# Kernel optimization log

Hardware: AMD Instinct MI355X
Metric: run time of the kernel (lower is better)

The kernel has to match this reference:

```python
import jax, jax.numpy as jnp
import numpy as np

WINDOW = (7, 7)
SHIFT = (3, 3)
NUM_HEADS = 4
DIM = 128


def _rel_pos_index():
    wh, ww = WINDOW
    coords = np.stack(np.meshgrid(np.arange(wh), np.arange(ww), indexing='ij'))  # [2,wh,ww]
    cf = coords.reshape(2, -1)                    # [2, N]
    rc = (cf[:, :, None] - cf[:, None, :]).transpose(1, 2, 0)  # [N,N,2]
    rc[:, :, 0] += wh - 1
    rc[:, :, 1] += ww - 1
    rc[:, :, 0] *= 2 * ww - 1
    return jnp.asarray(rc.sum(-1).reshape(-1))    # [N*N] int


def _attn_mask_np(pH, pW, sh):
    # Static-shape shift mask (host-side numpy; constant under jit).
    wh, ww = WINDOW
    m = np.zeros((pH, pW))
    h_slices = ((0, pH - wh), (pH - wh, pH - sh[0]), (pH - sh[0], pH))
    w_slices = ((0, pW - ww), (pW - ww, pW - sh[1]), (pW - sh[1], pW))
    cnt = 0
    for hs in h_slices:
        for ws in w_slices:
            m[hs[0]:hs[1], ws[0]:ws[1]] = cnt
            cnt += 1
    m = m.reshape(pH // wh, wh, pW // ww, ww).transpose(0, 2, 1, 3).reshape(-1, wh * ww)
    diff = m[:, None, :] - m[:, :, None]          # [num_windows, N, N]
    return jnp.asarray(np.where(diff != 0, -100.0, 0.0), dtype=np.float32)


def setup_inputs() -> dict:
    key = jax.random.key(0)
    ks = jax.random.split(key, 9)
    B, H, W, C = 32, 56, 56, DIM
    return {
        'input_q': jax.random.normal(ks[0], (B, H, W, C), jnp.float32),
        'input_k': jax.random.normal(ks[1], (B, H, W, C), jnp.float32),
        'input_v': jax.random.normal(ks[2], (B, H, W, C), jnp.float32),
        'q_weight': jax.random.normal(ks[3], (C, C), jnp.float32) * 0.05,
        'q_bias': jnp.zeros((C,), jnp.float32),
        'k_weight': jax.random.normal(ks[4], (C, C), jnp.float32) * 0.05,
        'k_bias': jnp.zeros((C,), jnp.float32),
        'v_weight': jax.random.normal(ks[5], (C, C), jnp.float32) * 0.05,
        'v_bias': jnp.zeros((C,), jnp.float32),
        'proj_weight': jax.random.normal(ks[6], (C, C), jnp.float32) * 0.05,
        'proj_bias': jnp.zeros((C,), jnp.float32),
        'rpb_table': jax.random.normal(ks[7], ((2 * WINDOW[0] - 1) * (2 * WINDOW[1] - 1), NUM_HEADS), jnp.float32) * 0.02,
    }


def reference(input_q, input_k, input_v, q_weight, q_bias, k_weight, k_bias,
              v_weight, v_bias, proj_weight, proj_bias, rpb_table):
    B, H, W, C = input_q.shape
    wh, ww = WINDOW
    pad_b = (wh - H % wh) % wh
    pad_r = (ww - W % ww) % ww
    pad = lambda t: jnp.pad(t, ((0, 0), (0, pad_b), (0, pad_r), (0, 0)))
    qx, kx, vx = pad(input_q), pad(input_k), pad(input_v)
    pad_H, pad_W = H + pad_b, W + pad_r
    sh = [0 if wh >= pad_H else SHIFT[0], 0 if ww >= pad_W else SHIFT[1]]
    if sum(sh) > 0:
        roll = lambda t: jnp.roll(t, (-sh[0], -sh[1]), axis=(1, 2))
        qx, kx, vx = roll(qx), roll(kx), roll(vx)
    nWh, nWw = pad_H // wh, pad_W // ww
    num_windows = nWh * nWw
    N = wh * ww

    def part(t):  # [B,pH,pW,C] -> [B*num_windows, N, C]
        t = t.reshape(B, nWh, wh, nWw, ww, C).transpose(0, 1, 3, 2, 4, 5)
        return t.reshape(B * num_windows, N, C)

    qx, kx, vx = part(qx), part(kx), part(vx)
    hd = C // NUM_HEADS

    def heads(x, w, b):  # linear + split heads -> [BW, nH, N, hd]
        return (x @ w.T + b).reshape(-1, N, NUM_HEADS, hd).transpose(0, 2, 1, 3)

    q = heads(qx, q_weight, q_bias) * (hd ** -0.5)
    k = heads(kx, k_weight, k_bias)
    v = heads(vx, v_weight, v_bias)

    attn = jnp.einsum('whqd,whkd->whqk', q, k)    # [BW, nH, N, N]
    rpb = rpb_table[_rel_pos_index()].reshape(N, N, NUM_HEADS).transpose(2, 0, 1)[None]
    attn = attn + rpb
    if sum(sh) > 0:
        mask = _attn_mask_np(pad_H, pad_W, sh)    # [num_windows, N, N]
        attn = attn.reshape(B, num_windows, NUM_HEADS, N, N) + mask[None, :, None]
        attn = attn.reshape(B * num_windows, NUM_HEADS, N, N)
    attn = jax.nn.softmax(attn, axis=-1)

    x = jnp.einsum('whqk,whkd->whqd', attn, v).transpose(0, 2, 1, 3).reshape(B * num_windows, N, C)
    x = x @ proj_weight.T + proj_bias
    x = x.reshape(B, nWh, nWw, wh, ww, C).transpose(0, 1, 3, 2, 4, 5).reshape(B, pad_H, pad_W, C)
    if sum(sh) > 0:
        x = jnp.roll(x, (sh[0], sh[1]), axis=(1, 2))
    return x[:, :H, :W, :]
```

## Files before the change

### kernel.cpp

```cpp
#include <hip/hip_runtime.h>
#include <hip/hip_bf16.h>

typedef __attribute__((ext_vector_type(8))) short s16x8;
typedef __attribute__((ext_vector_type(4))) float f32x4;
typedef __attribute__((ext_vector_type(2))) unsigned int u32x2;
typedef __attribute__((ext_vector_type(4))) unsigned int u32x4;

#define MFMA16(a, b, c) __builtin_amdgcn_mfma_f32_16x16x32_bf16((a), (b), (c), 0, 0, 0)
#define LOG2E 1.4426950408889634f

static __device__ __forceinline__ unsigned int pk2(float a, float b) {
  union { __hip_bfloat162 h2; unsigned int u; } cv;
  cv.h2 = __float22bfloat162_rn(make_float2(a, b));
  return cv.u;
}
static __device__ __forceinline__ int div7(int x) { return (x * 9363) >> 16; }
static __device__ __forceinline__ int swz256(int row, int byteoff) {
  return row * 256 + (byteoff ^ ((row & 7) << 4));
}
static __device__ __forceinline__ int swz128(int row, int byteoff) {
  return row * 128 + (byteoff ^ ((row & 7) << 4));
}

__global__ void swin_prep(const float* __restrict__ wq, const float* __restrict__ wk,
                          const float* __restrict__ wv, const float* __restrict__ wp,
                          const float* __restrict__ rpb_table,
                          unsigned short* __restrict__ wsW, float* __restrict__ rpbm) {
  int idx = blockIdx.x * 256 + threadIdx.x;
  if (idx < 65536) {
    int t = idx >> 14, loc = idx & 16383;
    const float* s = (t == 0) ? wq : (t == 1) ? wk : (t == 2) ? wv : wp;
    union { __hip_bfloat16 h; unsigned short u; } cv;
    cv.h = __float2bfloat16(s[loc]);
    wsW[idx] = cv.u;
  } else {
    int k = idx - 65536;
    int c = k >> 14;
    int h = (k >> 12) & 3;
    int i = (k >> 6) & 63, j = k & 63;
    float val;
    if (j >= 49) val = -1e30f;
    else if (i >= 49) val = 0.f;
    else {
      int yi = div7(i), xi = i - yi * 7;
      int yj = div7(j), xj = j - yj * 7;
      int ridx = (yi - yj + 6) * 13 + (xi - xj + 6);
      val = rpb_table[ridx * 4 + h];
      int cwi = c >> 1, cwj = c & 1;
      int rgi = (cwi ? (yi < 4 ? 3 : 6) : 0) + (cwj ? (xi < 4 ? 1 : 2) : 0);
      int rgj = (cwi ? (yj < 4 ? 3 : 6) : 0) + (cwj ? (xj < 4 ? 1 : 2) : 0);
      if (rgi != rgj) val -= 100.f;
      val *= LOG2E;
    }
    rpbm[k] = val;
  }
}

__global__ __launch_bounds__(512, 4) void swin_main(
    const float* __restrict__ xq, const float* __restrict__ xk, const float* __restrict__ xv,
    const float* __restrict__ bq, const float* __restrict__ bk, const float* __restrict__ bv,
    const float* __restrict__ bp, const unsigned short* __restrict__ wsW,
    const float* __restrict__ rpbm, float* __restrict__ out) {
  __shared__ __align__(16) char sm[65536];

  const int tid = threadIdx.x;
  const int lane = tid & 63;
  const int wv_ = tid >> 6;
  const int l15 = lane & 15;
  const int lg = lane >> 4;
  const int kgrp = lg * 8;
  const int rsub = lg * 4;

  const int bid = blockIdx.x;
  const int b = bid >> 6;
  const int widx = bid & 63;
  const int wi = widx >> 3, wj = widx & 7;
  const long obase = (long)b * 56 * 56 * 128;
  const int mcase = ((wi == 7) ? 2 : 0) + ((wj == 7) ? 1 : 0);

  const int xrow = tid >> 3;
  const int xk16 = (tid & 7) << 4;
  long xoff = -1;
  if (xrow < 49) {
    int ty = div7(xrow), tx = xrow - ty * 7;
    int ih = wi * 7 + ty + 3; if (ih >= 56) ih -= 56;
    int iw = wj * 7 + tx + 3; if (iw >= 56) iw -= 56;
    xoff = obase + (long)((ih * 56 + iw) * 128 + xk16);
  }
  float xr[16];
#pragma unroll
  for (int i = 0; i < 16; ++i) xr[i] = 0.f;

  auto issue_x = [&](const float* src) {
    if (xoff >= 0) {
      const float* p = src + xoff;
#pragma unroll
      for (int q = 0; q < 4; ++q) {
        f32x4 v = *(const f32x4*)(p + q * 4);
        xr[q * 4 + 0] = v[0]; xr[q * 4 + 1] = v[1];
        xr[q * 4 + 2] = v[2]; xr[q * 4 + 3] = v[3];
      }
    }
  };
  auto write_x = [&]() {
    unsigned int w[8];
#pragma unroll
    for (int i = 0; i < 8; ++i) w[i] = pk2(xr[2 * i], xr[2 * i + 1]);
    u32x4 a = {w[0], w[1], w[2], w[3]};
    u32x4 bb = {w[4], w[5], w[6], w[7]};
    *(u32x4*)(sm + swz256(xrow, xk16 * 2)) = a;
    *(u32x4*)(sm + swz256(xrow, xk16 * 2 + 16)) = bb;
  };
  auto st2 = [&](int a0, int a1, float v0, float v1) {
    unsigned int u = pk2(v0, v1);
    *(unsigned short*)(sm + a0) = (unsigned short)u;
    *(unsigned short*)(sm + a1) = (unsigned short)(u >> 16);
  };

  auto linearT = [&](int woff, const float* bias, float scale, int dstbase) {
    const int nrow = wv_ * 16 + l15;
    s16x8 afr[4];
#pragma unroll
    for (int kt = 0; kt < 4; ++kt)
      afr[kt] = *(const s16x8*)(wsW + woff + nrow * 128 + kt * 32 + kgrp);
    f32x4 bv4 = *(const f32x4*)(bias + wv_ * 16 + rsub);
    float bb0 = bv4[0] * scale, bb1 = bv4[1] * scale;
    float bb2 = bv4[2] * scale, bb3 = bv4[3] * scale;
#pragma unroll
    for (int tt = 0; tt < 4; ++tt) {
      f32x4 acc = {0.f, 0.f, 0.f, 0.f};
#pragma unroll
      for (int kt = 0; kt < 4; ++kt) {
        s16x8 bfr = *(const s16x8*)(sm + swz256(tt * 16 + l15, (kt * 32 + kgrp) * 2));
        acc = MFMA16(afr[kt], bfr, acc);
      }
      u32x2 pkw = {pk2(acc[0] * scale + bb0, acc[1] * scale + bb1),
                   pk2(acc[2] * scale + bb2, acc[3] * scale + bb3)};
      *(u32x2*)(sm + dstbase + swz256(tt * 16 + l15, 2 * (wv_ * 16 + rsub))) = pkw;
    }
  };

  auto linearV = [&](int woff, const float* bias) {
    const int n = wv_ * 16 + l15;
    s16x8 bfr[4];
#pragma unroll
    for (int kt = 0; kt < 4; ++kt)
      bfr[kt] = *(const s16x8*)(wsW + woff + n * 128 + kt * 32 + kgrp);
    float bval = bias[n];
#pragma unroll
    for (int mt = 0; mt < 4; ++mt) {
      f32x4 acc = {0.f, 0.f, 0.f, 0.f};
#pragma unroll
      for (int kt = 0; kt < 4; ++kt) {
        s16x8 afr = *(const s16x8*)(sm + swz256(mt * 16 + l15, (kt * 32 + kgrp) * 2));
        acc = MFMA16(afr, bfr[kt], acc);
      }
      u32x2 pkw = {pk2(acc[0] + bval, acc[1] + bval), pk2(acc[2] + bval, acc[3] + bval)};
      *(u32x2*)(sm + 49152 + swz128(n, 2 * (mt * 16 + rsub))) = pkw;
    }
  };

  const float QSCALE = 0.17677669529663687f * LOG2E;

  issue_x(xq);
  write_x(); __syncthreads();
  issue_x(xk);
  linearT(0, bq, QSCALE, 16384); __syncthreads();
  write_x(); __syncthreads();
  issue_x(xv);
  linearT(16384, bk, 1.f, 32768); __syncthreads();
  write_x(); __syncthreads();

  const int h = wv_ & 3;
  const int half = wv_ >> 2;
  const int coff = h * 32;
  f32x4 S[2][4];
  {
    linearV(32768, bv);

    const float* rpbm_h = rpbm + (((mcase << 2) + h) << 12);
    float rv[2][4][4];
#pragma unroll
    for (int m2 = 0; m2 < 2; ++m2)
#pragma unroll
      for (int r = 0; r < 4; ++r) {
        int i = (half * 2 + m2) * 16 + rsub + r;
        const float* rp = rpbm_h + i * 64 + l15;
#pragma unroll
        for (int jt = 0; jt < 4; ++jt) rv[m2][jt][r] = rp[jt * 16];
      }

    s16x8 kfr[4];
#pragma unroll
    for (int jt = 0; jt < 4; ++jt)
      kfr[jt] = *(const s16x8*)(sm + 32768 + swz256(jt * 16 + l15, (coff + kgrp) * 2));
#pragma unroll
    for (int m2 = 0; m2 < 2; ++m2) {
      int mt = half * 2 + m2;
      s16x8 qfr = *(const s16x8*)(sm + 16384 + swz256(mt * 16 + l15, (coff + kgrp) * 2));
#pragma unroll
      for (int jt = 0; jt < 4; ++jt) {
        f32x4 z = {0.f, 0.f, 0.f, 0.f};
        S[m2][jt] = MFMA16(qfr, kfr[jt], z);
      }
    }

#pragma unroll
    for (int m2 = 0; m2 < 2; ++m2)
#pragma unroll
      for (int jt = 0; jt < 4; ++jt)
#pragma unroll
        for (int r = 0; r < 4; ++r) S[m2][jt][r] += rv[m2][jt][r];

#pragma unroll
    for (int m2 = 0; m2 < 2; ++m2) {
#pragma unroll
      for (int r = 0; r < 4; ++r) {
        float m = fmaxf(fmaxf(S[m2][0][r], S[m2][1][r]), fmaxf(S[m2][2][r], S[m2][3][r]));
        for (int d = 1; d < 16; d <<= 1) m = fmaxf(m, __shfl_xor(m, d));
        float e0 = exp2f(S[m2][0][r] - m);
        float e1 = exp2f(S[m2][1][r] - m);
        float e2 = exp2f(S[m2][2][r] - m);
        float e3 = exp2f(S[m2][3][r] - m);
        float s = e0 + e1 + e2 + e3;
        for (int d = 1; d < 16; d <<= 1) s += __shfl_xor(s, d);
        float inv = 1.0f / s;
        S[m2][0][r] = e0 * inv; S[m2][1][r] = e1 * inv;
        S[m2][2][r] = e2 * inv; S[m2][3][r] = e3 * inv;
      }
    }
  }
  __syncthreads();

  const int pbase = 16384 + h * 8192;
#pragma unroll
  for (int m2 = 0; m2 < 2; ++m2) {
    int i0 = (half * 2 + m2) * 16 + rsub;
#pragma unroll
    for (int jt = 0; jt < 4; ++jt) {
      int bo = 2 * (jt * 16 + l15);
      st2(pbase + swz128(i0, bo), pbase + swz128(i0 + 1, bo), S[m2][jt][0], S[m2][jt][1]);
      st2(pbase + swz128(i0 + 2, bo), pbase + swz128(i0 + 3, bo), S[m2][jt][2], S[m2][jt][3]);
    }
  }
  __syncthreads();

  {
    s16x8 vfr[2][2];
#pragma unroll
    for (int ks = 0; ks < 2; ++ks)
#pragma unroll
      for (int ct = 0; ct < 2; ++ct) {
        int c = coff + ct * 16 + l15;
        vfr[ks][ct] = *(const s16x8*)(sm + 49152 + swz128(c, (ks * 32 + kgrp) * 2));
      }
    f32x4 Oacc[2][2];
#pragma unroll
    for (int ct = 0; ct < 2; ++ct)
#pragma unroll
      for (int qt = 0; qt < 2; ++qt) Oacc[ct][qt] = (f32x4){0.f, 0.f, 0.f, 0.f};
#pragma unroll
    for (int qt = 0; qt < 2; ++qt) {
#pragma unroll
      for (int ks = 0; ks < 2; ++ks) {
        s16x8 pfr = *(const s16x8*)(sm + pbase + swz128((half * 2 + qt) * 16 + l15, (ks * 32 + kgrp) * 2));
        Oacc[0][qt] = MFMA16(vfr[ks][0], pfr, Oacc[0][qt]);
        Oacc[1][qt] = MFMA16(vfr[ks][1], pfr, Oacc[1][qt]);
      }
    }
#pragma unroll
    for (int ct = 0; ct < 2; ++ct)
#pragma unroll
      for (int qt = 0; qt < 2; ++qt) {
        int qtok = (half * 2 + qt) * 16 + l15;
        u32x2 pkw = {pk2(Oacc[ct][qt][0], Oacc[ct][qt][1]),
                     pk2(Oacc[ct][qt][2], Oacc[ct][qt][3])};
        *(u32x2*)(sm + swz256(qtok, 2 * (coff + ct * 16 + rsub))) = pkw;
      }
  }
  __syncthreads();

  {
    const int nrow = wv_ * 16 + l15;
    s16x8 afr[4];
#pragma unroll
    for (int kt = 0; kt < 4; ++kt)
      afr[kt] = *(const s16x8*)(wsW + 49152 + nrow * 128 + kt * 32 + kgrp);
    f32x4 bv4 = *(const f32x4*)(bp + wv_ * 16 + rsub);
#pragma unroll
    for (int tt = 0; tt < 4; ++tt) {
      f32x4 acc = {0.f, 0.f, 0.f, 0.f};
#pragma unroll
      for (int kt = 0; kt < 4; ++kt) {
        s16x8 bfr = *(const s16x8*)(sm + swz256(tt * 16 + l15, (kt * 32 + kgrp) * 2));
        acc = MFMA16(afr[kt], bfr, acc);
      }
      int tok = tt * 16 + l15;
      if (tok < 49) {
        int ty = div7(tok), tx = tok - ty * 7;
        int oh = wi * 7 + ty + 3; if (oh >= 56) oh -= 56;
        int ow = wj * 7 + tx + 3; if (ow >= 56) ow -= 56;
        f32x4 res = {acc[0] + bv4[0], acc[1] + bv4[1], acc[2] + bv4[2], acc[3] + bv4[3]};
        *(f32x4*)(out + obase + (oh * 56 + ow) * 128 + wv_ * 16 + rsub) = res;
      }
    }
  }
}

extern "C" void kernel_launch(void* const* d_in, const int* in_sizes, int n_in,
                              void* d_out, int out_size, void* d_ws, size_t ws_size,
                              hipStream_t stream) {
  const float* xq = (const float*)d_in[0];
  const float* xk = (const float*)d_in[1];
  const float* xv = (const float*)d_in[2];
  const float* wq = (const float*)d_in[3];
  const float* bq = (const float*)d_in[4];
  const float* wk = (const float*)d_in[5];
  const float* bk = (const float*)d_in[6];
  const float* wv = (const float*)d_in[7];
  const float* bv = (const float*)d_in[8];
  const float* wp = (const float*)d_in[9];
  const float* bp = (const float*)d_in[10];
  const float* rpb = (const float*)d_in[11];

  unsigned short* wsW = (unsigned short*)d_ws;
  float* rpbm = (float*)((char*)d_ws + 131072);

  swin_prep<<<512, 256, 0, stream>>>(wq, wk, wv, wp, rpb, wsW, rpbm);

  float* out = (float*)d_out;
  swin_main<<<2048, 512, 0, stream>>>(xq, xk, xv, bq, bk, bv, bp, wsW, rpbm, out);
}
```

Baseline: 81.39 us.

## Use 32x32 MFMA for attention, keep P in registers, shrink LDS

Rewrites the QK^T and PV stages to use 32x32x16 MFMA with transposed S so each lane owns a query row, doing softmax mostly in-lane with one cross-half shuffle. The probabilities stay in registers and are exchanged via shuffles instead of going through LDS. The V projection is moved after the softmax so buffers can be reused, cutting shared memory from 64KB to 48KB and raising the occupancy hint to 6 blocks. This risks extra register pressure and an added barrier reshuffle.

```diff
diff --git a/kernel.cpp b/kernel.cpp
--- a/kernel.cpp
+++ b/kernel.cpp
@@ -3,10 +3,12 @@
 
 typedef __attribute__((ext_vector_type(8))) short s16x8;
 typedef __attribute__((ext_vector_type(4))) float f32x4;
+typedef __attribute__((ext_vector_type(16))) float f32x16;
 typedef __attribute__((ext_vector_type(2))) unsigned int u32x2;
 typedef __attribute__((ext_vector_type(4))) unsigned int u32x4;
 
 #define MFMA16(a, b, c) __builtin_amdgcn_mfma_f32_16x16x32_bf16((a), (b), (c), 0, 0, 0)
+#define MFMA32(a, b, c) __builtin_amdgcn_mfma_f32_32x32x16_bf16((a), (b), (c), 0, 0, 0)
 #define LOG2E 1.4426950408889634f
 
 static __device__ __forceinline__ unsigned int pk2(float a, float b) {
@@ -56,12 +58,12 @@
   }
 }
 
-__global__ __launch_bounds__(512, 4) void swin_main(
+__global__ __launch_bounds__(512, 6) void swin_main(
     const float* __restrict__ xq, const float* __restrict__ xk, const float* __restrict__ xv,
     const float* __restrict__ bq, const float* __restrict__ bk, const float* __restrict__ bv,
     const float* __restrict__ bp, const unsigned short* __restrict__ wsW,
     const float* __restrict__ rpbm, float* __restrict__ out) {
-  __shared__ __align__(16) char sm[65536];
+  __shared__ __align__(16) char sm[49152];
 
   const int tid = threadIdx.x;
   const int lane = tid & 63;
@@ -70,6 +72,8 @@
   const int lg = lane >> 4;
   const int kgrp = lg * 8;
   const int rsub = lg * 4;
+  const int l31 = lane & 31;
+  const int hi = lane >> 5;
 
   const int bid = blockIdx.x;
   const int b = bid >> 6;
@@ -111,11 +115,6 @@
     *(u32x4*)(sm + swz256(xrow, xk16 * 2)) = a;
     *(u32x4*)(sm + swz256(xrow, xk16 * 2 + 16)) = bb;
   };
-  auto st2 = [&](int a0, int a1, float v0, float v1) {
-    unsigned int u = pk2(v0, v1);
-    *(unsigned short*)(sm + a0) = (unsigned short)u;
-    *(unsigned short*)(sm + a1) = (unsigned short)(u >> 16);
-  };
 
   auto linearT = [&](int woff, const float* bias, float scale, int dstbase) {
     const int nrow = wv_ * 16 + l15;
@@ -156,7 +155,7 @@
         acc = MFMA16(afr, bfr[kt], acc);
       }
       u32x2 pkw = {pk2(acc[0] + bval, acc[1] + bval), pk2(acc[2] + bval, acc[3] + bval)};
-      *(u32x2*)(sm + 49152 + swz128(n, 2 * (mt * 16 + rsub))) = pkw;
+      *(u32x2*)(sm + 16384 + swz128(n, 2 * (mt * 16 + rsub))) = pkw;
     }
   };
 
@@ -169,114 +168,80 @@
   write_x(); __syncthreads();
   issue_x(xv);
   linearT(16384, bk, 1.f, 32768); __syncthreads();
-  write_x(); __syncthreads();
+  write_x();
 
   const int h = wv_ & 3;
   const int half = wv_ >> 2;
   const int coff = h * 32;
-  f32x4 S[2][4];
+  unsigned int pu[2][4][2];
   {
-    linearV(32768, bv);
-
-    const float* rpbm_h = rpbm + (((mcase << 2) + h) << 12);
-    float rv[2][4][4];
-#pragma unroll
-    for (int m2 = 0; m2 < 2; ++m2)
-#pragma unroll
-      for (int r = 0; r < 4; ++r) {
-        int i = (half * 2 + m2) * 16 + rsub + r;
-        const float* rp = rpbm_h + i * 64 + l15;
-#pragma unroll
-        for (int jt = 0; jt < 4; ++jt) rv[m2][jt][r] = rp[jt * 16];
-      }
-
-    s16x8 kfr[4];
-#pragma unroll
-    for (int jt = 0; jt < 4; ++jt)
-      kfr[jt] = *(const s16x8*)(sm + 32768 + swz256(jt * 16 + l15, (coff + kgrp) * 2));
-#pragma unroll
-    for (int m2 = 0; m2 < 2; ++m2) {
-      int mt = half * 2 + m2;
-      s16x8 qfr = *(const s16x8*)(sm + 16384 + swz256(mt * 16 + l15, (coff + kgrp) * 2));
-#pragma unroll
-      for (int jt = 0; jt < 4; ++jt) {
-        f32x4 z = {0.f, 0.f, 0.f, 0.f};
-        S[m2][jt] = MFMA16(qfr, kfr[jt], z);
-      }
-    }
-
-#pragma unroll
-    for (int m2 = 0; m2 < 2; ++m2)
-#pragma unroll
-      for (int jt = 0; jt < 4; ++jt)
-#pragma unroll
-        for (int r = 0; r < 4; ++r) S[m2][jt][r] += rv[m2][jt][r];
-
-#pragma unroll
-    for (int m2 = 0; m2 < 2; ++m2) {
-#pragma unroll
-      for (int r = 0; r < 4; ++r) {
-        float m = fmaxf(fmaxf(S[m2][0][r], S[m2][1][r]), fmaxf(S[m2][2][r], S[m2][3][r]));
-        for (int d = 1; d < 16; d <<= 1) m = fmaxf(m, __shfl_xor(m, d));
-        float e0 = exp2f(S[m2][0][r] - m);
-        float e1 = exp2f(S[m2][1][r] - m);
-        float e2 = exp2f(S[m2][2][r] - m);
-        float e3 = exp2f(S[m2][3][r] - m);
-        float s = e0 + e1 + e2 + e3;
-        for (int d = 1; d < 16; d <<= 1) s += __shfl_xor(s, d);
-        float inv = 1.0f / s;
-        S[m2][0][r] = e0 * inv; S[m2][1][r] = e1 * inv;
-        S[m2][2][r] = e2 * inv; S[m2][3][r] = e3 * inv;
-      }
-    }
+    s16x8 qfr[2], kfr[2][2];
+#pragma unroll
+    for (int s = 0; s < 2; ++s) {
+      qfr[s] = *(const s16x8*)(sm + 16384 + swz256(half * 32 + l31, 2 * (coff + s * 16 + hi * 8)));
+#pragma unroll
+      for (int t = 0; t < 2; ++t)
+        kfr[t][s] = *(const s16x8*)(sm + 32768 + swz256(t * 32 + l31, 2 * (coff + s * 16 + hi * 8)));
+    }
+    f32x16 S[2];
+    S[0] = (f32x16)0.f; S[1] = (f32x16)0.f;
+#pragma unroll
+    for (int s = 0; s < 2; ++s) {
+      S[0] = MFMA32(kfr[0][s], qfr[s], S[0]);
+      S[1] = MFMA32(kfr[1][s], qfr[s], S[1]);
+    }
+    const float* rpbm_h = rpbm + (((mcase << 2) + h) << 12) + (half * 32 + l31) * 64 + 4 * hi;
+#pragma unroll
+    for (int t = 0; t < 2; ++t)
+#pragma unroll
+      for (int g = 0; g < 4; ++g) {
+        f32x4 rv = *(const f32x4*)(rpbm_h + t * 32 + g * 8);
+#pragma unroll
+        for (int e = 0; e < 4; ++e) S[t][g * 4 + e] += rv[e];
+      }
+    float m = S[0][0];
+#pragma unroll
+    for (int t = 0; t < 2; ++t)
+#pragma unroll
+      for (int r = 0; r < 16; ++r) m = fmaxf(m, S[t][r]);
+    m = fmaxf(m, __shfl_xor(m, 32));
+    float sum = 0.f;
+#pragma unroll
+    for (int t = 0; t < 2; ++t)
+#pragma unroll
+      for (int r = 0; r < 16; ++r) { float e = exp2f(S[t][r] - m); S[t][r] = e; sum += e; }
+    sum += __shfl_xor(sum, 32);
+    float inv = 1.0f / sum;
+#pragma unroll
+    for (int t = 0; t < 2; ++t)
+#pragma unroll
+      for (int g = 0; g < 4; ++g) {
+        pu[t][g][0] = pk2(S[t][g * 4 + 0] * inv, S[t][g * 4 + 1] * inv);
+        pu[t][g][1] = pk2(S[t][g * 4 + 2] * inv, S[t][g * 4 + 3] * inv);
+      }
   }
   __syncthreads();
-
-  const int pbase = 16384 + h * 8192;
-#pragma unroll
-  for (int m2 = 0; m2 < 2; ++m2) {
-    int i0 = (half * 2 + m2) * 16 + rsub;
-#pragma unroll
-    for (int jt = 0; jt < 4; ++jt) {
-      int bo = 2 * (jt * 16 + l15);
-      st2(pbase + swz128(i0, bo), pbase + swz128(i0 + 1, bo), S[m2][jt][0], S[m2][jt][1]);
-      st2(pbase + swz128(i0 + 2, bo), pbase + swz128(i0 + 3, bo), S[m2][jt][2], S[m2][jt][3]);
-    }
-  }
+  linearV(32768, bv);
   __syncthreads();
 
   {
-    s16x8 vfr[2][2];
-#pragma unroll
-    for (int ks = 0; ks < 2; ++ks)
-#pragma unroll
-      for (int ct = 0; ct < 2; ++ct) {
-        int c = coff + ct * 16 + l15;
-        vfr[ks][ct] = *(const s16x8*)(sm + 49152 + swz128(c, (ks * 32 + kgrp) * 2));
-      }
-    f32x4 Oacc[2][2];
-#pragma unroll
-    for (int ct = 0; ct < 2; ++ct)
-#pragma unroll
-      for (int qt = 0; qt < 2; ++qt) Oacc[ct][qt] = (f32x4){0.f, 0.f, 0.f, 0.f};
-#pragma unroll
-    for (int qt = 0; qt < 2; ++qt) {
-#pragma unroll
-      for (int ks = 0; ks < 2; ++ks) {
-        s16x8 pfr = *(const s16x8*)(sm + pbase + swz128((half * 2 + qt) * 16 + l15, (ks * 32 + kgrp) * 2));
-        Oacc[0][qt] = MFMA16(vfr[ks][0], pfr, Oacc[0][qt]);
-        Oacc[1][qt] = MFMA16(vfr[ks][1], pfr, Oacc[1][qt]);
-      }
-    }
-#pragma unroll
-    for (int ct = 0; ct < 2; ++ct)
-#pragma unroll
-      for (int qt = 0; qt < 2; ++qt) {
-        int qtok = (half * 2 + qt) * 16 + l15;
-        u32x2 pkw = {pk2(Oacc[ct][qt][0], Oacc[ct][qt][1]),
-                     pk2(Oacc[ct][qt][2], Oacc[ct][qt][3])};
-        *(u32x2*)(sm + swz256(qtok, 2 * (coff + ct * 16 + rsub))) = pkw;
-      }
+    f32x16 O = (f32x16)0.f;
+#pragma unroll
+    for (int s = 0; s < 4; ++s) {
+      const int t = s >> 1, gb = (s & 1) * 2;
+      unsigned int own0 = pu[t][gb + hi][0], own1 = pu[t][gb + hi][1];
+      unsigned int po0 = __shfl_xor(pu[t][gb + 1 - hi][0], 32);
+      unsigned int po1 = __shfl_xor(pu[t][gb + 1 - hi][1], 32);
+      union { u32x4 u; s16x8 s; } pf;
+      pf.u = hi ? (u32x4){po0, po1, own0, own1} : (u32x4){own0, own1, po0, po1};
+      s16x8 vfr = *(const s16x8*)(sm + 16384 + swz128(coff + l31, 2 * (s * 16 + hi * 8)));
+      O = MFMA32(vfr, pf.s, O);
+    }
+#pragma unroll
+    for (int g = 0; g < 4; ++g) {
+      u32x2 w = {pk2(O[g * 4 + 0], O[g * 4 + 1]), pk2(O[g * 4 + 2], O[g * 4 + 3])};
+      *(u32x2*)(sm + 32768 + swz256(half * 32 + l31, 2 * (coff + g * 8 + 4 * hi))) = w;
+    }
   }
   __syncthreads();
 
@@ -292,7 +257,7 @@
       f32x4 acc = {0.f, 0.f, 0.f, 0.f};
 #pragma unroll
       for (int kt = 0; kt < 4; ++kt) {
-        s16x8 bfr = *(const s16x8*)(sm + swz256(tt * 16 + l15, (kt * 32 + kgrp) * 2));
+        s16x8 bfr = *(const s16x8*)(sm + 32768 + swz256(tt * 16 + l15, (kt * 32 + kgrp) * 2));
         acc = MFMA16(afr[kt], bfr, acc);
       }
       int tok = tt * 16 + l15;
```

Result: slower. 87.01 us (+6.9%).
